# Performance work log

Measured on AMD Instinct MI355X. Metric: run time of the kernel, lower is better.

The kernel has to match this reference:

```python
import jax, jax.numpy as jnp
import numpy as np

N, D, H, C, E, M = 8192, 256, 256, 64, 262144, 2048
WD = 5e-4   # weight_decay
HP1 = 0.9
TAU = 0.5


def _l2norm(x, eps=1e-12):
    n = jnp.sqrt(jnp.sum(x * x, axis=1, keepdims=True))
    return x / jnp.maximum(n, eps)


def setup_inputs() -> dict:
    key = jax.random.key(0)
    ks = jax.random.split(key, 20)
    s = 0.05
    return dict(
        features=jax.random.uniform(ks[0], (N, D), dtype=jnp.float32),
        support=jax.random.uniform(ks[1], (N, N), dtype=jnp.float32) / N,  # mimics normalized adjacency scale
        labels=jax.random.uniform(ks[2], (N, C), dtype=jnp.float32),
        mat01_intra=jax.random.uniform(ks[3], (M, M), dtype=jnp.float32),
        mat01_inter=jax.random.uniform(ks[4], (M, M), dtype=jnp.float32),
        W0=jax.random.normal(ks[5], (D, H), dtype=jnp.float32) * s,
        b0=jnp.zeros((H,), jnp.float32),
        W1=jax.random.normal(ks[6], (H, C), dtype=jnp.float32) * s,
        b1=jnp.zeros((C,), jnp.float32),
        Wh0=jax.random.normal(ks[7], (D, H), dtype=jnp.float32) * s,
        bh0=jnp.zeros((H,), jnp.float32),
        Wh1=jax.random.normal(ks[8], (H, C), dtype=jnp.float32) * s,
        bh1=jnp.zeros((C,), jnp.float32),
        Wc=jax.random.normal(ks[9], (2 * C, 1), dtype=jnp.float32) * s,
        bc=jnp.zeros((1,), jnp.float32),
        edge_pos_i=jax.random.randint(ks[10], (E,), 0, N, dtype=jnp.int32),
        edge_pos_j=jax.random.randint(ks[11], (E,), 0, N, dtype=jnp.int32),
        train_idx=jax.random.randint(ks[12], (M,), 0, N, dtype=jnp.int32),
        mask=jax.random.randint(ks[13], (N,), 0, 2, dtype=jnp.int32),
    )


def _forward(features, support, labels, mat01_intra, mat01_inter,
             W0, b0, W1, b1, Wh0, bh0, Wh1, bh1, Wc, bc,
             edge_pos_i, edge_pos_j, train_idx, mask):
    # --- GCN branch: relu(S (X W0) + b0) -> S (h0 W1) + b1
    h0 = jax.nn.relu(support @ (features @ W0) + b0)
    h1 = support @ (h0 @ W1) + b1
    gcn_n = _l2norm(h1)
    # --- HGCN branch (2-layer GCN stand-in)
    g0 = jax.nn.relu(support @ (features @ Wh0) + bh0)
    hgcn = support @ (g0 @ Wh1) + bh1
    hgcn_n = _l2norm(hgcn)
    outputs = _l2norm(0.6 * gcn_n + 0.4 * hgcn_n)

    # masked softmax cross entropy
    maskf = mask.astype(jnp.float32)
    maskf = maskf / jnp.mean(maskf)
    logp = jax.nn.log_softmax(outputs, axis=1)
    loss_ce = jnp.mean(-jnp.sum(labels * logp, axis=1) * maskf)

    # edge gathers + contra MLP: log sigmoid of linear on concatenated pairs
    yi_g, yj_g = gcn_n[edge_pos_i], gcn_n[edge_pos_j]
    yi_h, yj_h = hgcn_n[edge_pos_i], hgcn_n[edge_pos_j]
    z1 = jnp.concatenate([yi_g, yj_h], axis=1) @ Wc + bc  # [E,1]
    z2 = jnp.concatenate([yi_h, yj_g], axis=1) @ Wc + bc
    p_e_xy = -jnp.mean(jax.nn.log_sigmoid(z1)) - jnp.mean(jax.nn.log_sigmoid(z2))

    # unsupervised contrastive over full NxN
    cd1 = jnp.exp((gcn_n @ hgcn_n.T) / TAU)      # [N,N]
    pn1 = jnp.diagonal(cd1) / jnp.mean(cd1, axis=1)
    cd2 = jnp.exp((hgcn_n @ gcn_n.T) / TAU)
    pn2 = jnp.diagonal(cd2) / jnp.mean(cd2, axis=1)
    contra = -HP1 * jnp.mean(jnp.log(jnp.concatenate([pn1, pn2], axis=0)))

    # supervised contrastive on train subset
    rowsum = jnp.sum(mat01_intra, axis=1)  # mat01_intra_rowsum buffer
    h1t, h2t = gcn_n[train_idx], hgcn_n[train_idx]
    Mn = train_idx.shape[0]

    def sup(a, b):
        hc = jnp.exp((a @ b.T) / TAU)            # [M,M]
        sp = jnp.sum(hc * mat01_intra, axis=1)
        sn = (jnp.sum(hc * mat01_inter, axis=1) + sp) / (Mn - 1)
        return (sp / rowsum) / sn

    pns = jnp.concatenate([sup(h1t, h2t), sup(h2t, h1t)], axis=0)
    contra = contra + (-HP1 * jnp.mean(jnp.log(pns)))

    wd = WD * 0.5 * (jnp.sum(W0 ** 2) + jnp.sum(b0 ** 2) + jnp.sum(W1 ** 2)
                     + jnp.sum(b1 ** 2) + jnp.sum(Wc ** 2) + jnp.sum(bc ** 2))
    loss = loss_ce + 0.4 * p_e_xy + contra + wd  # HGCN.loss = 0 for the stand-in

    correct = (jnp.argmax(outputs, axis=1) == jnp.argmax(labels, axis=1)).astype(jnp.float32)
    accuracy = jnp.mean(correct * maskf)
    return outputs, loss, accuracy


def reference(features, support, labels, mat01_intra, mat01_inter,
              W0, b0, W1, b1, Wh0, bh0, Wh1, bh1, Wc, bc,
              edge_pos_i, edge_pos_j, train_idx, mask):
    return _forward(features, support, labels, mat01_intra, mat01_inter,
                    W0, b0, W1, b1, Wh0, bh0, Wh1, bh1, Wc, bc,
                    edge_pos_i, edge_pos_j, train_idx, mask)
```

## Files before the change

### kernel.cpp

```cpp
#include <hip/hip_runtime.h>

#define DEVI __device__ __forceinline__

typedef __bf16 bf16x8 __attribute__((ext_vector_type(8)));
typedef float f32x4 __attribute__((ext_vector_type(4)));
typedef unsigned short u16;
typedef unsigned long long ull;

constexpr int NN = 8192;
constexpr int EE = 262144;

constexpr size_t OF_WT0b = 0;
constexpr size_t OF_WT1b = OF_WT0b + 65536;
constexpr size_t OF_BIA0 = OF_WT1b + 32768;
constexpr size_t OF_X16  = OF_BIA0 + 512;
constexpr size_t OF_A    = OF_X16 + 1048576;
constexpr size_t OF_B    = OF_A + 2097152;
constexpr size_t OF_C    = OF_B + 2097152;
constexpr size_t OF_D    = OF_C + 2097152;
constexpr size_t OF_VEC  = OF_D + 524288;
constexpr size_t OF_SD   = OF_VEC;
constexpr size_t OF_R1   = OF_SD + 8192;
constexpr size_t OF_R2   = OF_R1 + 16384;
constexpr size_t OF_AG   = OF_R2 + 16384;
constexpr size_t OF_BG   = OF_AG + 8192;
constexpr size_t OF_AH   = OF_BG + 8192;
constexpr size_t OF_BH   = OF_AH + 8192;
constexpr size_t OF_SP1  = OF_BH + 8192;
constexpr size_t OF_SNR1 = OF_SP1 + 2048;
constexpr size_t OF_SP2  = OF_SNR1 + 2048;
constexpr size_t OF_SNR2 = OF_SP2 + 2048;
constexpr size_t OF_RSI  = OF_SNR2 + 2048;
constexpr size_t OF_SCAL = OF_RSI + 2048;
constexpr size_t WS_SMALL = OF_SCAL + 16;
constexpr size_t OF_S16  = WS_SMALL;
constexpr size_t WS_FULL = OF_S16 + 16777216;

#define SC_CE 0
#define SC_MASK 1
#define SC_ACC 2
#define SC_E1 3
#define SC_E2 4
#define SC_C1 5
#define SC_C2 6
#define SC_WD 7

DEVI u16 bf1(float f) { __bf16 h = (__bf16)f; return __builtin_bit_cast(u16, h); }
DEVI unsigned int bf2(float a, float b) {
  return (unsigned)bf1(a) | ((unsigned)bf1(b) << 16);
}
DEVI ull bf4(float4 v) {
  return (ull)bf2(v.x, v.y) | ((ull)bf2(v.z, v.w) << 32);
}
DEVI float b2f(u16 h) { return __uint_as_float(((unsigned)h) << 16); }
DEVI float lo16(unsigned w) { return __uint_as_float(w << 16); }
DEVI float hi16(unsigned w) { return __uint_as_float(w & 0xffff0000u); }
DEVI f32x4 mfma16(bf16x8 a, bf16x8 b, f32x4 c) {
  return __builtin_amdgcn_mfma_f32_16x16x32_bf16(a, b, c, 0, 0, 0);
}
DEVI float wsum64(float v) {
  #pragma unroll
  for (int m = 1; m < 64; m <<= 1) v += __shfl_xor(v, m, 64);
  return v;
}
DEVI float wmax64(float v) {
  #pragma unroll
  for (int m = 1; m < 64; m <<= 1) v = fmaxf(v, __shfl_xor(v, m, 64));
  return v;
}
DEVI int wargmax64(float v, int idx) {
  #pragma unroll
  for (int m = 1; m < 64; m <<= 1) {
    float ov = __shfl_xor(v, m, 64);
    int   oi = __shfl_xor(idx, m, 64);
    if (ov > v || (ov == v && oi < idx)) { v = ov; idx = oi; }
  }
  return idx;
}
DEVI void blockAtomicAdd(float* dst, float v) {
  __shared__ float red[4];
  const int tid = threadIdx.x;
  v = wsum64(v);
  __syncthreads();
  if ((tid & 63) == 0) red[tid >> 6] = v;
  __syncthreads();
  if (tid == 0) atomicAdd(dst, red[0] + red[1] + red[2] + red[3]);
}
DEVI float logsig(float z) {
  return fminf(z, 0.f) - log1pf(__expf(-fabsf(z)));
}

__global__ __launch_bounds__(256)
void cvtbf(const float* __restrict__ src, u16* __restrict__ dst, long n8) {
  long stride = (long)gridDim.x * 256;
  for (long i = (long)blockIdx.x * 256 + threadIdx.x; i < n8; i += stride) {
    long off = i << 3;
    float4 a = *(const float4*)(src + off);
    float4 b = *(const float4*)(src + off + 4);
    uint4 o;
    o.x = bf2(a.x, a.y); o.y = bf2(a.z, a.w);
    o.z = bf2(b.x, b.y); o.w = bf2(b.z, b.w);
    *(uint4*)(dst + off) = o;
  }
}

__global__ void prep(const float* __restrict__ W0, const float* __restrict__ Wh0,
                     const float* __restrict__ W1, const float* __restrict__ Wh1,
                     const float* __restrict__ b0, const float* __restrict__ bh0,
                     u16* __restrict__ wt0, u16* __restrict__ wt1,
                     float* __restrict__ bias0) {
  int t = blockIdx.x * 256 + threadIdx.x;
  if (t < 131072) {
    int j = t >> 8, k = t & 255;
    wt0[t] = bf1((j < 256) ? W0[k * 256 + j] : Wh0[k * 256 + (j - 256)]);
  } else if (t < 196608) {
    int u = t - 131072;
    int j = u >> 9, k = u & 511;
    float v = 0.f;
    if (j < 64)  { if (k < 256)  v = W1 [k * 64 + j]; }
    else         { if (k >= 256) v = Wh1[(k - 256) * 64 + (j - 64)]; }
    wt1[u] = bf1(v);
  } else if (t < 197120) {
    int j = t - 196608;
    bias0[j] = (j < 256) ? b0[j] : bh0[j - 256];
  }
}

template <int FM, int FN, int SWZ, int MLOC, int NLOG, int MINB>
__global__ __launch_bounds__(256, MINB)
void gemm_a(const u16* __restrict__ A16, const u16* __restrict__ B16,
            u16* __restrict__ Cv, int K, int Ntot, int ksteps, size_t splitStride) {
  constexpr int BM = 32 * FM, BN = 32 * FN;
  constexpr int NSEG = (BM + BN) / 16;
  constexpr int SPW = NSEG / 4;
  __shared__ __align__(16) u16 As[2][BM * 32];
  __shared__ __align__(16) u16 Bs[2][BN * 32];
  const int tid = threadIdx.x;
  const int l = tid & 63, wid = tid >> 6;
  const int wr = wid >> 1, wc = wid & 1;
  const int fr = l & 15, fg = l >> 4;

  int m0, n0;
  if (SWZ) {
    int id = blockIdx.x + gridDim.x * blockIdx.y;
    int e = id & 7, s = id >> 3;
    m0 = (e * MLOC + (s >> NLOG)) * BM;
    n0 = (s & ((1 << NLOG) - 1)) * BN;
  } else {
    m0 = blockIdx.y * BM;
    n0 = blockIdx.x * BN;
  }
  const size_t kbase = (size_t)blockIdx.z * ksteps * 32;

  const u16* gsrc[SPW];
  u16* ld0[SPW];
  u16* ld1[SPW];
  #pragma unroll
  for (int q = 0; q < SPW; ++q) {
    int s = q * 4 + wid;
    if (s < BM / 16) {
      gsrc[q] = A16 + (size_t)(m0 + s * 16 + (l & 15)) * K + kbase + ((l >> 4) << 3);
      ld0[q] = &As[0][s << 9];
      ld1[q] = &As[1][s << 9];
    } else {
      int t2 = s - BM / 16;
      gsrc[q] = B16 + (size_t)(n0 + t2 * 16 + (l & 15)) * K + kbase + ((l >> 4) << 3);
      ld0[q] = &Bs[0][t2 << 9];
      ld1[q] = &Bs[1][t2 << 9];
    }
  }
  auto stageTo = [&](int buf, int ks2) {
    int koff = ks2 * 32;
    #pragma unroll
    for (int q = 0; q < SPW; ++q) {
      u16* d = buf ? ld1[q] : ld0[q];
      __builtin_amdgcn_global_load_lds(
          (const __attribute__((address_space(1))) void*)(gsrc[q] + koff),
          (__attribute__((address_space(3))) void*)d, 16, 0, 0);
    }
  };

  f32x4 zero = {0.f, 0.f, 0.f, 0.f};
  f32x4 acc[FM][FN];
  #pragma unroll
  for (int i = 0; i < FM; ++i)
    #pragma unroll
    for (int j = 0; j < FN; ++j) acc[i][j] = zero;

  stageTo(0, 0);
  int cur = 0;
  for (int ks = 0; ks < ksteps; ++ks) {
    __syncthreads();
    if (ks + 1 < ksteps) stageTo(cur ^ 1, ks + 1);
    bf16x8 af[FM], bfv[FN];
    #pragma unroll
    for (int i = 0; i < FM; ++i)
      af[i] = *(const bf16x8*)&As[cur][((wr * FM + i) << 9) + (l << 3)];
    #pragma unroll
    for (int j = 0; j < FN; ++j)
      bfv[j] = *(const bf16x8*)&Bs[cur][((wc * FN + j) << 9) + (l << 3)];
    #pragma unroll
    for (int i = 0; i < FM; ++i)
      #pragma unroll
      for (int j = 0; j < FN; ++j)
        acc[i][j] = mfma16(af[i], bfv[j], acc[i][j]);
    cur ^= 1;
  }

  u16* outp = Cv + (size_t)blockIdx.z * splitStride;
  #pragma unroll
  for (int i = 0; i < FM; ++i)
    #pragma unroll
    for (int j = 0; j < FN; ++j)
      #pragma unroll
      for (int r = 0; r < 4; ++r) {
        int grow = m0 + wr * 16 * FM + i * 16 + (fg << 2) + r;
        int gcol = n0 + wc * 16 * FN + j * 16 + fr;
        outp[(size_t)grow * Ntot + gcol] = bf1(acc[i][j][r]);
      }
}

template <int FM, int FN, int TA, int TB, int SWZ, int MLOC, int NLOG, int MINB>
__global__ __launch_bounds__(256, MINB)
void gemm_k(const void* __restrict__ Av, const void* __restrict__ Bv,
            u16* __restrict__ Cv, int K, int Ntot, int ksteps, size_t splitStride) {
  constexpr int BM = 32 * FM, BN = 32 * FN;
  constexpr int PAf = BM / 32, PAh = BM / 64 > 0 ? BM / 64 : 1;
  constexpr int PBf = BN / 32, PBh = BN / 64 > 0 ? BN / 64 : 1;
  __shared__ __align__(16) u16 As[2][BM * 32];
  __shared__ __align__(16) u16 Bs[2][BN * 32];
  const int tid = threadIdx.x;
  const int l = tid & 63, wid = tid >> 6;
  const int wr = wid >> 1, wc = wid & 1;
  const int fr = l & 15, fg = l >> 4;

  int m0, n0;
  if (SWZ) {
    int id = blockIdx.x + gridDim.x * blockIdx.y;
    int e = id & 7, s = id >> 3;
    m0 = (e * MLOC + (s >> NLOG)) * BM;
    n0 = (s & ((1 << NLOG) - 1)) * BN;
  } else {
    m0 = blockIdx.y * BM;
    n0 = blockIdx.x * BN;
  }
  const size_t kbase = (size_t)blockIdx.z * ksteps * 32;

  float4 ra32[TA ? 1 : PAf];
  uint4  ra16[TA ? PAh : 1];
  float4 rb32[TB ? 1 : PBf];
  uint4  rb16[TB ? PBh : 1];

  auto loadT = [&](int koff) {
    if constexpr (!TA) {
      #pragma unroll
      for (int p = 0; p < PAf; ++p) {
        int idx = p * 256 + tid;
        int lane = (idx & 127) >> 1, half = idx & 1;
        int row = ((idx >> 7) << 4) + (lane & 15);
        int kcol = ((lane >> 4) << 3) + (half << 2);
        ra32[p] = *(const float4*)((const float*)Av + (size_t)(m0 + row) * K + kbase + koff + kcol);
      }
    } else {
      #pragma unroll
      for (int p = 0; p < PAh; ++p) {
        int idx = p * 256 + tid;
        int lane = idx & 63;
        int row = ((idx >> 6) << 4) + (lane & 15);
        int kcol = (lane >> 4) << 3;
        ra16[p] = *(const uint4*)((const u16*)Av + (size_t)(m0 + row) * K + kbase + koff + kcol);
      }
    }
    if constexpr (!TB) {
      #pragma unroll
      for (int p = 0; p < PBf; ++p) {
        int idx = p * 256 + tid;
        int lane = (idx & 127) >> 1, half = idx & 1;
        int row = ((idx >> 7) << 4) + (lane & 15);
        int kcol = ((lane >> 4) << 3) + (half << 2);
        rb32[p] = *(const float4*)((const float*)Bv + (size_t)(n0 + row) * K + kbase + koff + kcol);
      }
    } else {
      #pragma unroll
      for (int p = 0; p < PBh; ++p) {
        int idx = p * 256 + tid;
        int lane = idx & 63;
        int row = ((idx >> 6) << 4) + (lane & 15);
        int kcol = (lane >> 4) << 3;
        rb16[p] = *(const uint4*)((const u16*)Bv + (size_t)(n0 + row) * K + kbase + koff + kcol);
      }
    }
  };
  auto writeT = [&](int buf) {
    if constexpr (!TA) {
      #pragma unroll
      for (int p = 0; p < PAf; ++p) {
        int idx = p * 256 + tid;
        *(ull*)&As[buf][idx << 2] = bf4(ra32[p]);
      }
    } else {
      #pragma unroll
      for (int p = 0; p < PAh; ++p) {
        int idx = p * 256 + tid;
        *(uint4*)&As[buf][idx << 3] = ra16[p];
      }
    }
    if constexpr (!TB) {
      #pragma unroll
      for (int p = 0; p < PBf; ++p) {
        int idx = p * 256 + tid;
        *(ull*)&Bs[buf][idx << 2] = bf4(rb32[p]);
      }
    } else {
      #pragma unroll
      for (int p = 0; p < PBh; ++p) {
        int idx = p * 256 + tid;
        *(uint4*)&Bs[buf][idx << 3] = rb16[p];
      }
    }
  };

  f32x4 zero = {0.f, 0.f, 0.f, 0.f};
  f32x4 acc[FM][FN];
  #pragma unroll
  for (int i = 0; i < FM; ++i)
    #pragma unroll
    for (int j = 0; j < FN; ++j) acc[i][j] = zero;

  loadT(0);
  writeT(0);
  if (ksteps > 1) loadT(32);
  __syncthreads();

  for (int ks = 0; ks < ksteps; ++ks) {
    const int cur = ks & 1;
    bf16x8 af[FM], bfv[FN];
    #pragma unroll
    for (int i = 0; i < FM; ++i)
      af[i] = *(const bf16x8*)&As[cur][((wr * FM + i) << 9) + (l << 3)];
    #pragma unroll
    for (int j = 0; j < FN; ++j)
      bfv[j] = *(const bf16x8*)&Bs[cur][((wc * FN + j) << 9) + (l << 3)];
    if (ks + 1 < ksteps) writeT(cur ^ 1);
    if (ks + 2 < ksteps) loadT((ks + 2) * 32);
    #pragma unroll
    for (int i = 0; i < FM; ++i)
      #pragma unroll
      for (int j = 0; j < FN; ++j)
        acc[i][j] = mfma16(af[i], bfv[j], acc[i][j]);
    __syncthreads();
  }

  u16* outp = Cv + (size_t)blockIdx.z * splitStride;
  #pragma unroll
  for (int i = 0; i < FM; ++i)
    #pragma unroll
    for (int j = 0; j < FN; ++j)
      #pragma unroll
      for (int r = 0; r < 4; ++r) {
        int grow = m0 + wr * 16 * FM + i * 16 + (fg << 2) + r;
        int gcol = n0 + wc * 16 * FN + j * 16 + fr;
        outp[(size_t)grow * Ntot + gcol] = bf1(acc[i][j][r]);
      }
}

__global__ __launch_bounds__(256)
void relupack(const u16* __restrict__ z0, const u16* __restrict__ z1,
              const float* __restrict__ bias, u16* __restrict__ h16) {
  int t = blockIdx.x * 256 + threadIdx.x;
  int off = t << 3;
  uint4 a = *(const uint4*)(z0 + off);
  uint4 b = *(const uint4*)(z1 + off);
  int col = off & 511;
  float4 c0 = *(const float4*)(bias + col);
  float4 c1 = *(const float4*)(bias + col + 4);
  float r0 = fmaxf(lo16(a.x) + lo16(b.x) + c0.x, 0.f);
  float r1 = fmaxf(hi16(a.x) + hi16(b.x) + c0.y, 0.f);
  float r2 = fmaxf(lo16(a.y) + lo16(b.y) + c0.z, 0.f);
  float r3 = fmaxf(hi16(a.y) + hi16(b.y) + c0.w, 0.f);
  float r4 = fmaxf(lo16(a.z) + lo16(b.z) + c1.x, 0.f);
  float r5 = fmaxf(hi16(a.z) + hi16(b.z) + c1.y, 0.f);
  float r6 = fmaxf(lo16(a.w) + lo16(b.w) + c1.z, 0.f);
  float r7 = fmaxf(hi16(a.w) + hi16(b.w) + c1.w, 0.f);
  uint4 o;
  o.x = bf2(r0, r1); o.y = bf2(r2, r3); o.z = bf2(r4, r5); o.w = bf2(r6, r7);
  *(uint4*)(h16 + off) = o;
}

__global__ __launch_bounds__(256)
void rowstats(const u16* __restrict__ Z2p, const float* __restrict__ b1,
              const float* __restrict__ bh1, const float* __restrict__ labels,
              const int* __restrict__ mask, const float* __restrict__ Wc,
              float* __restrict__ outp, u16* __restrict__ gcn16, u16* __restrict__ hgcn16,
              float* __restrict__ sd, float* __restrict__ ag, float* __restrict__ bg,
              float* __restrict__ ah, float* __restrict__ bh, float* __restrict__ scal) {
  const int tid = threadIdx.x, l = tid & 63, w = tid >> 6;
  const float wa = Wc[l], wb = Wc[64 + l];
  const float bb1 = b1[l], bbh1 = bh1[l];
  float s_ce = 0.f, s_mk = 0.f, s_ac = 0.f;
  for (int it = 0; it < 8; ++it) {
    int row = blockIdx.x * 32 + it * 4 + w;
    float h1 = bb1, hg = bbh1;
    #pragma unroll
    for (int s = 0; s < 8; ++s) {
      h1 += b2f(Z2p[(size_t)s * 1048576 + row * 128 + l]);
      hg += b2f(Z2p[(size_t)s * 1048576 + row * 128 + 64 + l]);
    }
    float n1 = wsum64(h1 * h1);
    float gn = h1 / fmaxf(sqrtf(n1), 1e-12f);
    float n2 = wsum64(hg * hg);
    float hn = hg / fmaxf(sqrtf(n2), 1e-12f);
    float oc = 0.6f * gn + 0.4f * hn;
    float n3 = wsum64(oc * oc);
    float o = oc / fmaxf(sqrtf(n3), 1e-12f);
    size_t ro = (size_t)row * 64 + l;
    outp[ro] = o; gcn16[ro] = bf1(gn); hgcn16[ro] = bf1(hn);
    float sdv = wsum64(gn * hn);
    float vag = wsum64(gn * wa), vbg = wsum64(gn * wb);
    float vah = wsum64(hn * wa), vbh = wsum64(hn * wb);
    float lab = labels[ro];
    float mx = wmax64(o);
    float se = wsum64(__expf(o - mx));
    float lse = mx + __logf(se);
    float slab = wsum64(lab);
    float slo = wsum64(lab * o);
    int am_o = wargmax64(o, l);
    int am_l = wargmax64(lab, l);
    if (l == 0) {
      sd[row] = sdv; ag[row] = vag; bg[row] = vbg; ah[row] = vah; bh[row] = vbh;
      float mk = (float)mask[row];
      s_ce += (lse * slab - slo) * mk;
      s_mk += mk;
      s_ac += (am_o == am_l) ? mk : 0.f;
    }
  }
  blockAtomicAdd(&scal[SC_CE], s_ce);
  blockAtomicAdd(&scal[SC_MASK], s_mk);
  blockAtomicAdd(&scal[SC_ACC], s_ac);
}

__global__ __launch_bounds__(256)
void rowsumexp2(const u16* __restrict__ G16, const u16* __restrict__ H16,
                float* __restrict__ R1, float* __restrict__ R2) {
  constexpr int PK = 72;
  __shared__ __align__(16) u16 At[64 * PK];
  __shared__ __align__(16) u16 Bt[64 * PK];
  const int bx = blockIdx.x;
  const int nh = bx >> 8, r = bx & 255, dir = r >> 7;
  const u16* __restrict__ A = dir ? H16 : G16;
  const u16* __restrict__ B = dir ? G16 : H16;
  float* __restrict__ out = (dir ? R2 : R1) + nh * 8192;
  const int tid = threadIdx.x, l = tid & 63, w = tid >> 6;
  const int m0 = (r & 127) * 64;
  #pragma unroll
  for (int p = 0; p < 2; ++p) {
    int idx = p * 256 + tid, row = idx >> 3, kq = (idx & 7) << 3;
    *(uint4*)&At[row * PK + kq] = *(const uint4*)(A + (size_t)(m0 + row) * 64 + kq);
  }
  __syncthreads();
  const int fr = l & 15, fg = l >> 4;
  bf16x8 a0 = *(const bf16x8*)&At[(w * 16 + fr) * PK + (fg << 3)];
  bf16x8 a1 = *(const bf16x8*)&At[(w * 16 + fr) * PK + 32 + (fg << 3)];
  float rs0 = 0.f, rs1 = 0.f, rs2 = 0.f, rs3 = 0.f;
  const int nbeg = nh * 4096;
  for (int n0 = nbeg; n0 < nbeg + 4096; n0 += 64) {
    __syncthreads();
    #pragma unroll
    for (int p = 0; p < 2; ++p) {
      int idx = p * 256 + tid, row = idx >> 3, kq = (idx & 7) << 3;
      *(uint4*)&Bt[row * PK + kq] = *(const uint4*)(B + (size_t)(n0 + row) * 64 + kq);
    }
    __syncthreads();
    #pragma unroll
    for (int jn = 0; jn < 4; ++jn) {
      bf16x8 b0 = *(const bf16x8*)&Bt[(jn * 16 + fr) * PK + (fg << 3)];
      bf16x8 b1 = *(const bf16x8*)&Bt[(jn * 16 + fr) * PK + 32 + (fg << 3)];
      f32x4 c = {0.f, 0.f, 0.f, 0.f};
      c = mfma16(a0, b0, c);
      c = mfma16(a1, b1, c);
      rs0 += __expf(c[0] * 2.0f);
      rs1 += __expf(c[1] * 2.0f);
      rs2 += __expf(c[2] * 2.0f);
      rs3 += __expf(c[3] * 2.0f);
    }
  }
  #pragma unroll
  for (int m = 1; m < 16; m <<= 1) {
    rs0 += __shfl_xor(rs0, m, 64);
    rs1 += __shfl_xor(rs1, m, 64);
    rs2 += __shfl_xor(rs2, m, 64);
    rs3 += __shfl_xor(rs3, m, 64);
  }
  if (fr == 0) {
    int rb = m0 + w * 16 + fg * 4;
    out[rb + 0] = rs0; out[rb + 1] = rs1; out[rb + 2] = rs2; out[rb + 3] = rs3;
  }
}

__global__ __launch_bounds__(256)
void supstats2(const u16* __restrict__ G16, const u16* __restrict__ H16,
               const int* __restrict__ tidx,
               const float* __restrict__ Wi_g, const float* __restrict__ We_g,
               float* __restrict__ SP1, float* __restrict__ SNR1,
               float* __restrict__ SP2, float* __restrict__ SNR2) {
  constexpr int PK = 72;
  __shared__ __align__(16) u16 At[64 * PK];
  __shared__ __align__(16) u16 Bt[64 * PK];
  __shared__ float Ws0[64 * 68];
  __shared__ float Ws1[64 * 68];
  const int bx = blockIdx.x;
  const int chunk = bx >> 6, sub = bx & 63, dir = sub >> 5;
  const u16* __restrict__ A = dir ? H16 : G16;
  const u16* __restrict__ B = dir ? G16 : H16;
  float* __restrict__ sp_out  = dir ? SP2 : SP1;
  float* __restrict__ sn_out  = dir ? SNR2 : SNR1;
  const int tid = threadIdx.x, l = tid & 63, w = tid >> 6;
  const int m0 = (sub & 31) * 64;
  #pragma unroll
  for (int p = 0; p < 2; ++p) {
    int idx = p * 256 + tid, row = idx >> 3, kq = (idx & 7) << 3;
    int gr = tidx[m0 + row];
    *(uint4*)&At[row * PK + kq] = *(const uint4*)(A + (size_t)gr * 64 + kq);
  }
  __syncthreads();
  const int fr = l & 15, fg = l >> 4;
  bf16x8 a0 = *(const bf16x8*)&At[(w * 16 + fr) * PK + (fg << 3)];
  bf16x8 a1 = *(const bf16x8*)&At[(w * 16 + fr) * PK + 32 + (fg << 3)];
  float sp0 = 0, sp1 = 0, sp2 = 0, sp3 = 0, sn0 = 0, sn1 = 0, sn2 = 0, sn3 = 0;
  const int nbeg = chunk * 512;
  for (int n0 = nbeg; n0 < nbeg + 512; n0 += 64) {
    __syncthreads();
    #pragma unroll
    for (int p = 0; p < 2; ++p) {
      int idx = p * 256 + tid, row = idx >> 3, kq = (idx & 7) << 3;
      int gr = tidx[n0 + row];
      *(uint4*)&Bt[row * PK + kq] = *(const uint4*)(B + (size_t)gr * 64 + kq);
    }
    #pragma unroll
    for (int p = 0; p < 4; ++p) {
      int idx = p * 256 + tid, row = idx >> 4, kq = (idx & 15) << 2;
      *(float4*)&Ws0[row * 68 + kq] = *(const float4*)(Wi_g + (size_t)(m0 + row) * 2048 + n0 + kq);
      *(float4*)&Ws1[row * 68 + kq] = *(const float4*)(We_g + (size_t)(m0 + row) * 2048 + n0 + kq);
    }
    __syncthreads();
    #pragma unroll
    for (int jn = 0; jn < 4; ++jn) {
      bf16x8 b0 = *(const bf16x8*)&Bt[(jn * 16 + fr) * PK + (fg << 3)];
      bf16x8 b1 = *(const bf16x8*)&Bt[(jn * 16 + fr) * PK + 32 + (fg << 3)];
      f32x4 c = {0.f, 0.f, 0.f, 0.f};
      c = mfma16(a0, b0, c);
      c = mfma16(a1, b1, c);
      int cl = jn * 16 + fr;
      int rl = w * 16 + fg * 4;
      float e0 = __expf(c[0] * 2.0f);
      float e1 = __expf(c[1] * 2.0f);
      float e2 = __expf(c[2] * 2.0f);
      float e3 = __expf(c[3] * 2.0f);
      sp0 += e0 * Ws0[(rl + 0) * 68 + cl]; sn0 += e0 * Ws1[(rl + 0) * 68 + cl];
      sp1 += e1 * Ws0[(rl + 1) * 68 + cl]; sn1 += e1 * Ws1[(rl + 1) * 68 + cl];
      sp2 += e2 * Ws0[(rl + 2) * 68 + cl]; sn2 += e2 * Ws1[(rl + 2) * 68 + cl];
      sp3 += e3 * Ws0[(rl + 3) * 68 + cl]; sn3 += e3 * Ws1[(rl + 3) * 68 + cl];
    }
  }
  #pragma unroll
  for (int m = 1; m < 16; m <<= 1) {
    sp0 += __shfl_xor(sp0, m, 64); sn0 += __shfl_xor(sn0, m, 64);
    sp1 += __shfl_xor(sp1, m, 64); sn1 += __shfl_xor(sn1, m, 64);
    sp2 += __shfl_xor(sp2, m, 64); sn2 += __shfl_xor(sn2, m, 64);
    sp3 += __shfl_xor(sp3, m, 64); sn3 += __shfl_xor(sn3, m, 64);
  }
  if (fr == 0) {
    int rb = m0 + w * 16 + fg * 4;
    atomicAdd(&sp_out[rb + 0], sp0); atomicAdd(&sn_out[rb + 0], sn0);
    atomicAdd(&sp_out[rb + 1], sp1); atomicAdd(&sn_out[rb + 1], sn1);
    atomicAdd(&sp_out[rb + 2], sp2); atomicAdd(&sn_out[rb + 2], sn2);
    atomicAdd(&sp_out[rb + 3], sp3); atomicAdd(&sn_out[rb + 3], sn3);
  }
}

__global__ __launch_bounds__(256)
void rowsum2048(const float* __restrict__ Wi, float* __restrict__ rsi) {
  int l = threadIdx.x & 63, w = threadIdx.x >> 6;
  int row = blockIdx.x * 4 + w;
  float s = 0.f;
  #pragma unroll
  for (int p = 0; p < 8; ++p) {
    int c = (p * 64 + l) << 2;
    float4 v = *(const float4*)(Wi + (size_t)row * 2048 + c);
    s += v.x + v.y + v.z + v.w;
  }
  s = wsum64(s);
  if (l == 0) rsi[row] = s;
}

__global__ __launch_bounds__(256)
void edgered(const int* __restrict__ ei, const int* __restrict__ ej,
             const float* __restrict__ ag, const float* __restrict__ bg,
             const float* __restrict__ ah, const float* __restrict__ bh,
             const float* __restrict__ bc, float* __restrict__ scal) {
  int t = blockIdx.x * 256 + threadIdx.x;
  float bcv = bc[0];
  float s1 = 0.f, s2 = 0.f;
  for (int e = t; e < EE; e += 65536) {
    int i = ei[e], j = ej[e];
    s1 += logsig(ag[i] + bh[j] + bcv);
    s2 += logsig(ah[i] + bg[j] + bcv);
  }
  blockAtomicAdd(&scal[SC_E1], s1);
  blockAtomicAdd(&scal[SC_E2], s2);
}

__global__ __launch_bounds__(256)
void contrared(const float* __restrict__ sd, const float* __restrict__ r1,
               const float* __restrict__ r2, float* __restrict__ scal) {
  int i = blockIdx.x * 256 + threadIdx.x;
  constexpr float LOGN = 9.01091334728f;
  float ra = r1[i] + r1[8192 + i];
  float rb = r2[i] + r2[8192 + i];
  float v = 4.f * sd[i] - __logf(ra) - __logf(rb) + 2.f * LOGN;
  blockAtomicAdd(&scal[SC_C1], v);
}

__global__ __launch_bounds__(256)
void supred(const float* __restrict__ sp1, const float* __restrict__ snr1,
            const float* __restrict__ sp2, const float* __restrict__ snr2,
            const float* __restrict__ rsi, float* __restrict__ scal) {
  int i = blockIdx.x * 256 + threadIdx.x;
  float rs = rsi[i];
  float a1 = sp1[i], d1 = (snr1[i] + a1) * (1.f / 2047.f);
  float a2 = sp2[i], d2 = (snr2[i] + a2) * (1.f / 2047.f);
  float v = __logf(a1 / rs / d1) + __logf(a2 / rs / d2);
  blockAtomicAdd(&scal[SC_C2], v);
}

__global__ __launch_bounds__(256)
void wdsum(const float* __restrict__ W0, const float* __restrict__ b0,
           const float* __restrict__ W1, const float* __restrict__ b1,
           const float* __restrict__ Wc, const float* __restrict__ bc,
           float* __restrict__ scal) {
  int t = threadIdx.x;
  float s = 0.f;
  for (int i = t; i < 16384; i += 256) {
    float4 v = *(const float4*)(W0 + i * 4);
    s += v.x * v.x + v.y * v.y + v.z * v.z + v.w * v.w;
  }
  for (int i = t; i < 4096; i += 256) {
    float4 v = *(const float4*)(W1 + i * 4);
    s += v.x * v.x + v.y * v.y + v.z * v.z + v.w * v.w;
  }
  if (t < 256) { float v = b0[t]; s += v * v; }
  if (t < 64)  { float v = b1[t]; s += v * v; }
  if (t < 128) { float v = Wc[t]; s += v * v; }
  if (t == 0)  { float v = bc[0]; s += v * v; }
  blockAtomicAdd(&scal[SC_WD], s);
}

__global__ void finalk(const float* __restrict__ scal, float* __restrict__ dst) {
  float masks = scal[SC_MASK];
  float loss = scal[SC_CE] / masks
             + 0.4f * (-(scal[SC_E1] + scal[SC_E2]) * (1.f / 262144.f))
             - 0.9f * scal[SC_C1] * (1.f / 16384.f)
             - 0.9f * scal[SC_C2] * (1.f / 4096.f)
             + 5e-4f * 0.5f * scal[SC_WD];
  dst[0] = loss;
  dst[1] = scal[SC_ACC] / masks;
}

extern "C" void kernel_launch(void* const* d_in, const int* in_sizes, int n_in,
                              void* d_out, int out_size, void* d_ws, size_t ws_size,
                              hipStream_t stream) {
  const float* features = (const float*)d_in[0];
  const float* support  = (const float*)d_in[1];
  const float* labels   = (const float*)d_in[2];
  const float* intra    = (const float*)d_in[3];
  const float* inter    = (const float*)d_in[4];
  const float* W0  = (const float*)d_in[5];
  const float* b0  = (const float*)d_in[6];
  const float* W1  = (const float*)d_in[7];
  const float* b1  = (const float*)d_in[8];
  const float* Wh0 = (const float*)d_in[9];
  const float* bh0 = (const float*)d_in[10];
  const float* Wh1 = (const float*)d_in[11];
  const float* bh1 = (const float*)d_in[12];
  const float* Wc  = (const float*)d_in[13];
  const float* bc  = (const float*)d_in[14];
  const int* ei    = (const int*)d_in[15];
  const int* ej    = (const int*)d_in[16];
  const int* tidx  = (const int*)d_in[17];
  const int* mask  = (const int*)d_in[18];

  if (ws_size < WS_SMALL * sizeof(float)) return;
  const bool big = ws_size >= WS_FULL * sizeof(float);

  float* ws = (float*)d_ws;
  u16*   WT0b  = (u16*)(ws + OF_WT0b);
  u16*   WT1b  = (u16*)(ws + OF_WT1b);
  float* BIA0  = ws + OF_BIA0;
  u16*   X16   = (u16*)(ws + OF_X16);
  u16*   XWT16 = (u16*)(ws + OF_A);
  u16*   H16   = (u16*)(ws + OF_A);
  u16*   ZbS0  = (u16*)(ws + OF_B);
  u16*   Z2p   = (u16*)(ws + OF_B);
  u16*   HWT16 = (u16*)(ws + OF_D);
  u16*   G16   = (u16*)(ws + OF_A);
  u16*   HG16  = (u16*)(ws + OF_A + 262144);
  u16*   S16   = (u16*)(ws + OF_S16);
  float* SD   = ws + OF_SD;
  float* R1   = ws + OF_R1;
  float* R2   = ws + OF_R2;
  float* AG   = ws + OF_AG;
  float* BG   = ws + OF_BG;
  float* AH   = ws + OF_AH;
  float* BH   = ws + OF_BH;
  float* SP1  = ws + OF_SP1;
  float* SNR1 = ws + OF_SNR1;
  float* SP2  = ws + OF_SP2;
  float* SNR2 = ws + OF_SNR2;
  float* RSI  = ws + OF_RSI;
  float* SCAL = ws + OF_SCAL;
  float* outp = (float*)d_out;

  hipMemsetAsync(SCAL, 0, 16 * sizeof(float), stream);
  hipMemsetAsync(SP1, 0, 4 * 2048 * sizeof(float), stream);
  prep<<<770, 256, 0, stream>>>(W0, Wh0, W1, Wh1, b0, bh0, WT0b, WT1b, BIA0);
  cvtbf<<<256, 256, 0, stream>>>(features, X16, 262144);

  gemm_a<4, 2, 0, 0, 0, 4><<<dim3(128, 4, 1), 256, 0, stream>>>(
      WT0b, X16, XWT16, 256, 8192, 8, 0);

  if (big) {
    cvtbf<<<4096, 256, 0, stream>>>(support, S16, 8388608);
    gemm_a<4, 2, 1, 8, 3, 4><<<dim3(8, 64, 2), 256, 0, stream>>>(
        S16, XWT16, ZbS0, 8192, 512, 128, (size_t)8192 * 512);
  } else {
    gemm_k<4, 4, 0, 1, 1, 8, 2, 3><<<dim3(4, 64, 2), 256, 0, stream>>>(
        support, XWT16, ZbS0, 8192, 512, 128, (size_t)8192 * 512);
  }

  relupack<<<2048, 256, 0, stream>>>(ZbS0, ZbS0 + (size_t)8192 * 512, BIA0, H16);

  gemm_a<2, 2, 0, 0, 0, 4><<<dim3(128, 2, 1), 256, 0, stream>>>(
      WT1b, H16, HWT16, 512, 8192, 16, 0);

  if (big) {
    gemm_a<4, 2, 1, 8, 1, 4><<<dim3(2, 64, 8), 256, 0, stream>>>(
        S16, HWT16, Z2p, 8192, 128, 32, (size_t)8192 * 128);
  } else {
    gemm_k<4, 4, 0, 1, 1, 8, 0, 3><<<dim3(1, 64, 8), 256, 0, stream>>>(
        support, HWT16, Z2p, 8192, 128, 32, (size_t)8192 * 128);
  }

  rowstats<<<256, 256, 0, stream>>>(Z2p, b1, bh1, labels, mask, Wc,
                                    outp, G16, HG16, SD, AG, BG, AH, BH, SCAL);
  rowsumexp2<<<512, 256, 0, stream>>>(G16, HG16, R1, R2);
  rowsum2048<<<512, 256, 0, stream>>>(intra, RSI);
  supstats2<<<256, 256, 0, stream>>>(G16, HG16, tidx, intra, inter,
                                     SP1, SNR1, SP2, SNR2);
  edgered<<<256, 256, 0, stream>>>(ei, ej, AG, BG, AH, BH, bc, SCAL);
  contrared<<<32, 256, 0, stream>>>(SD, R1, R2, SCAL);
  supred<<<8, 256, 0, stream>>>(SP1, SNR1, SP2, SNR2, RSI, SCAL);
  wdsum<<<1, 256, 0, stream>>>(W0, b0, W1, b1, Wc, bc, SCAL);
  finalk<<<1, 1, 0, stream>>>(SCAL, outp + (size_t)8192 * 64);
}
```

Baseline: 511.5 us.

## Deepen gemm_a LDS pipeline to four buffers with explicit vmcnt waits

The bf16 GEMM kernel moves from double-buffered to quad-buffered LDS staging, prefetching three k-steps ahead. The old __syncthreads is replaced by explicit s_waitcnt vmcnt counts plus a raw s_barrier, so the kernel waits only for the oldest stage. This hides more global-load latency in the support-matrix GEMMs. The larger LDS footprint costs occupancy, so min-blocks in launch_bounds drops from 4 to 3. The hand-counted waits depend on the compiler not reordering or adding other memory ops.

```diff
diff --git a/kernel.cpp b/kernel.cpp
--- a/kernel.cpp
+++ b/kernel.cpp
@@ -90,6 +90,15 @@
   return fminf(z, 0.f) - log1pf(__expf(-fabsf(z)));
 }
 
+template <int N> DEVI void vmwait() {
+  if constexpr (N == 0)      asm volatile("s_waitcnt vmcnt(0) lgkmcnt(0)" ::: "memory");
+  else if constexpr (N == 2) asm volatile("s_waitcnt vmcnt(2) lgkmcnt(0)" ::: "memory");
+  else if constexpr (N == 3) asm volatile("s_waitcnt vmcnt(3) lgkmcnt(0)" ::: "memory");
+  else if constexpr (N == 4) asm volatile("s_waitcnt vmcnt(4) lgkmcnt(0)" ::: "memory");
+  else if constexpr (N == 6) asm volatile("s_waitcnt vmcnt(6) lgkmcnt(0)" ::: "memory");
+  else                       asm volatile("s_waitcnt vmcnt(8) lgkmcnt(0)" ::: "memory");
+}
+
 __global__ __launch_bounds__(256)
 void cvtbf(const float* __restrict__ src, u16* __restrict__ dst, long n8) {
   long stride = (long)gridDim.x * 256;
@@ -133,8 +142,9 @@
   constexpr int BM = 32 * FM, BN = 32 * FN;
   constexpr int NSEG = (BM + BN) / 16;
   constexpr int SPW = NSEG / 4;
-  __shared__ __align__(16) u16 As[2][BM * 32];
-  __shared__ __align__(16) u16 Bs[2][BN * 32];
+  constexpr int ASZ = BM * 32, BSZ = BN * 32;
+  __shared__ __align__(16) u16 As[4][ASZ];
+  __shared__ __align__(16) u16 Bs[4][BSZ];
   const int tid = threadIdx.x;
   const int l = tid & 63, wid = tid >> 6;
   const int wr = wid >> 1, wc = wid & 1;
@@ -153,27 +163,27 @@
   const size_t kbase = (size_t)blockIdx.z * ksteps * 32;
 
   const u16* gsrc[SPW];
-  u16* ld0[SPW];
-  u16* ld1[SPW];
+  u16* ldb[SPW];
+  int  lstr[SPW];
   #pragma unroll
   for (int q = 0; q < SPW; ++q) {
     int s = q * 4 + wid;
     if (s < BM / 16) {
       gsrc[q] = A16 + (size_t)(m0 + s * 16 + (l & 15)) * K + kbase + ((l >> 4) << 3);
-      ld0[q] = &As[0][s << 9];
-      ld1[q] = &As[1][s << 9];
+      ldb[q] = &As[0][s << 9];
+      lstr[q] = ASZ;
     } else {
       int t2 = s - BM / 16;
       gsrc[q] = B16 + (size_t)(n0 + t2 * 16 + (l & 15)) * K + kbase + ((l >> 4) << 3);
-      ld0[q] = &Bs[0][t2 << 9];
-      ld1[q] = &Bs[1][t2 << 9];
+      ldb[q] = &Bs[0][t2 << 9];
+      lstr[q] = BSZ;
     }
   }
   auto stageTo = [&](int buf, int ks2) {
     int koff = ks2 * 32;
     #pragma unroll
     for (int q = 0; q < SPW; ++q) {
-      u16* d = buf ? ld1[q] : ld0[q];
+      u16* d = ldb[q] + buf * lstr[q];
       __builtin_amdgcn_global_load_lds(
           (const __attribute__((address_space(1))) void*)(gsrc[q] + koff),
           (__attribute__((address_space(3))) void*)d, 16, 0, 0);
@@ -187,11 +197,20 @@
     #pragma unroll
     for (int j = 0; j < FN; ++j) acc[i][j] = zero;
 
+  const int last = ksteps - 1;
   stageTo(0, 0);
-  int cur = 0;
+  if (ksteps > 1) stageTo(1, 1);
+  if (ksteps > 2) stageTo(2, 2);
+
   for (int ks = 0; ks < ksteps; ++ks) {
-    __syncthreads();
-    if (ks + 1 < ksteps) stageTo(cur ^ 1, ks + 1);
+    const int cur = ks & 3;
+    if (ks + 2 <= last)      vmwait<2 * SPW>();
+    else if (ks + 1 <= last) vmwait<SPW>();
+    else                     vmwait<0>();
+    __builtin_amdgcn_s_barrier();
+    asm volatile("" ::: "memory");
+    __builtin_amdgcn_sched_barrier(0);
+    if (ks + 3 <= last) stageTo((ks + 3) & 3, ks + 3);
     bf16x8 af[FM], bfv[FN];
     #pragma unroll
     for (int i = 0; i < FM; ++i)
@@ -204,7 +223,6 @@
       #pragma unroll
       for (int j = 0; j < FN; ++j)
         acc[i][j] = mfma16(af[i], bfv[j], acc[i][j]);
-    cur ^= 1;
   }
 
   u16* outp = Cv + (size_t)blockIdx.z * splitStride;
@@ -725,12 +743,12 @@
   prep<<<770, 256, 0, stream>>>(W0, Wh0, W1, Wh1, b0, bh0, WT0b, WT1b, BIA0);
   cvtbf<<<256, 256, 0, stream>>>(features, X16, 262144);
 
-  gemm_a<4, 2, 0, 0, 0, 4><<<dim3(128, 4, 1), 256, 0, stream>>>(
+  gemm_a<4, 2, 0, 0, 0, 3><<<dim3(128, 4, 1), 256, 0, stream>>>(
       WT0b, X16, XWT16, 256, 8192, 8, 0);
 
   if (big) {
     cvtbf<<<4096, 256, 0, stream>>>(support, S16, 8388608);
-    gemm_a<4, 2, 1, 8, 3, 4><<<dim3(8, 64, 2), 256, 0, stream>>>(
+    gemm_a<4, 2, 1, 8, 3, 3><<<dim3(8, 64, 2), 256, 0, stream>>>(
         S16, XWT16, ZbS0, 8192, 512, 128, (size_t)8192 * 512);
   } else {
     gemm_k<4, 4, 0, 1, 1, 8, 2, 3><<<dim3(4, 64, 2), 256, 0, stream>>>(
@@ -739,11 +757,11 @@
 
   relupack<<<2048, 256, 0, stream>>>(ZbS0, ZbS0 + (size_t)8192 * 512, BIA0, H16);
 
-  gemm_a<2, 2, 0, 0, 0, 4><<<dim3(128, 2, 1), 256, 0, stream>>>(
+  gemm_a<2, 2, 0, 0, 0, 3><<<dim3(128, 2, 1), 256, 0, stream>>>(
       WT1b, H16, HWT16, 512, 8192, 16, 0);
 
   if (big) {
-    gemm_a<4, 2, 1, 8, 1, 4><<<dim3(2, 64, 8), 256, 0, stream>>>(
+    gemm_a<4, 2, 1, 8, 1, 3><<<dim3(2, 64, 8), 256, 0, stream>>>(
         S16, HWT16, Z2p, 8192, 128, 32, (size_t)8192 * 128);
   } else {
     gemm_k<4, 4, 0, 1, 1, 8, 0, 3><<<dim3(1, 64, 8), 256, 0, stream>>>(
```

Result: slower. 596.7 us (+16.7%).
